# Performance work log

Measured on AMD Instinct MI355X. Metric: run time of the kernel, lower is better.

The kernel has to match this reference:

```python
import jax, jax.numpy as jnp
import numpy as np

TAU = 2.0
EPS = 1e-5
NUM_HEADS = 8


def _atan_surrogate(alpha):
    @jax.custom_vjp
    def f(x):
        return (x >= 0).astype(x.dtype)
    def fwd(x):
        return f(x), x
    def bwd(x, g):
        d = (alpha / 2.0) / (1.0 + (jnp.pi / 2.0 * alpha * x) ** 2)
        return (g * d,)
    f.defvjp(fwd, bwd)
    return f


def _sigmoid_surrogate(alpha):
    @jax.custom_vjp
    def f(x):
        return (x >= 0).astype(x.dtype)
    def fwd(x):
        return f(x), x
    def bwd(x, g):
        s = jax.nn.sigmoid(alpha * x)
        return (g * alpha * s * (1.0 - s),)
    f.defvjp(fwd, bwd)
    return f


spike_atan5 = _atan_surrogate(5.0)   # surrogate.ATan(alpha=5.0)
spike_sig4 = _sigmoid_surrogate(4.0)  # spikingjelly default surrogate.Sigmoid(alpha=4.0)


def lif(x, spike_fn, v_th=1.0):
    """LIF over leading time dim. decay_input=True, v_reset=0 (hard reset), detach_reset=True.
    x: [T, ...] membrane input. Returns spikes [T, ...]."""
    def step(v, xt):
        v = v + (xt - v) / TAU
        s = spike_fn(v - v_th)
        v = v * (1.0 - jax.lax.stop_gradient(s))  # hard reset to 0, detached
        return v, s
    _, spikes = jax.lax.scan(step, jnp.zeros_like(x[0]), x)
    return spikes


def conv1x1(x, w, b=None):
    # x: [T,B,Cin,H,W], w: [Cout,Cin]
    y = jnp.einsum('tbihw,oi->tbohw', x, w)
    if b is not None:
        y = y + b[None, None, :, None, None]
    return y


def bn(x, p):
    # eval-mode BatchNorm2d; p: [4,C] = (gamma, beta, running_mean, running_var)
    g, be, m, v = p[0], p[1], p[2], p[3]
    sc = g / jnp.sqrt(v + EPS)
    return (x - m[None, None, :, None, None]) * sc[None, None, :, None, None] + be[None, None, :, None, None]


def setup_inputs() -> dict:
    key = jax.random.key(0)
    T, B, C, H, W = 4, 16, 512, 16, 16
    hid = 4 * C
    ks = jax.random.split(key, 16)

    def w(k, o, i):
        return (jax.random.normal(k, (o, i), dtype=jnp.float32) / np.sqrt(i)).astype(jnp.float32)

    def make_bn(k, c):
        k1, k2, k3, k4 = jax.random.split(k, 4)
        g = 1.0 + 0.1 * jax.random.normal(k1, (c,), dtype=jnp.float32)
        be = 0.1 * jax.random.normal(k2, (c,), dtype=jnp.float32)
        m = 0.1 * jax.random.normal(k3, (c,), dtype=jnp.float32)
        v = 1.0 + 0.1 * jax.random.uniform(k4, (c,), dtype=jnp.float32)
        return jnp.stack([g, be, m, v])

    return {
        'x': jax.random.normal(ks[0], (T, B, C, H, W), dtype=jnp.float32),
        'q_w': w(ks[1], C, C), 'k_w': w(ks[2], C, C), 'v_w': w(ks[3], C, C),
        'proj_w': w(ks[4], C, C),
        'proj_b': 0.01 * jax.random.normal(ks[5], (C,), dtype=jnp.float32),
        'fc1_w': w(ks[6], hid, C),
        'fc1_b': 0.01 * jax.random.normal(ks[7], (hid,), dtype=jnp.float32),
        'fc2_w': w(ks[8], C, hid),
        'fc2_b': 0.01 * jax.random.normal(ks[9], (C,), dtype=jnp.float32),
        'q_bn': make_bn(ks[10], C), 'k_bn': make_bn(ks[11], C), 'v_bn': make_bn(ks[12], C),
        'proj_bn': make_bn(ks[13], C), 'fc1_bn': make_bn(ks[14], hid), 'fc2_bn': make_bn(ks[15], C),
    }


def reference(x, q_w, k_w, v_w, proj_w, proj_b, fc1_w, fc1_b, fc2_w, fc2_b,
              q_bn, k_bn, v_bn, proj_bn, fc1_bn, fc2_bn):
    T, B, C, H, W = x.shape
    N = H * W
    Ch = C // NUM_HEADS

    # ---- MS_SSA_Conv ----
    identity = x
    xs = lif(x, spike_sig4)                               # shortcut_lif (default surrogate)
    q = lif(bn(conv1x1(xs, q_w), q_bn), spike_atan5)      # [T,B,C,H,W] spikes
    k = lif(bn(conv1x1(xs, k_w), k_bn), spike_atan5)
    v = lif(bn(conv1x1(xs, v_w), v_bn), spike_atan5)

    def to_heads(t):  # [T,B,C,H,W] -> [T,B,h,N,Ch]
        return t.reshape(T, B, NUM_HEADS, Ch, N).transpose(0, 1, 2, 4, 3)

    qh, kh, vh = to_heads(q), to_heads(k), to_heads(v)
    kv = (kh * vh).sum(axis=3, keepdims=True)             # [T,B,h,1,Ch] linear attention reduce
    kv = lif(kv, spike_sig4, v_th=0.5)                    # talking_heads_lif
    att = qh * kv                                         # [T,B,h,N,Ch]
    att = att.transpose(0, 1, 2, 4, 3).reshape(T, B, C, H, W)
    x_attn = bn(conv1x1(att, proj_w, proj_b), proj_bn) + identity

    # ---- MS_MLP_Conv (hidden = 4*C != C, so no mid residual) ----
    idm = x_attn
    h = lif(x_attn, spike_atan5)
    h = bn(conv1x1(h, fc1_w, fc1_b), fc1_bn)              # [T,B,4C,H,W]
    h = lif(h, spike_atan5)
    h = bn(conv1x1(h, fc2_w, fc2_b), fc2_bn)
    out = h + idm
    return out, vh
```

## Files before the change

### kernel.cpp

```cpp
#include <hip/hip_runtime.h>
#include <stdint.h>

#pragma clang fp contract(off)

typedef int i32x4 __attribute__((ext_vector_type(4)));
typedef float f32x4 __attribute__((ext_vector_type(4)));
typedef unsigned char u8;

#define T_   4
#define B_   16
#define C_   512
#define HID_ 2048
#define NPIX 256
#define Z_   64

constexpr size_t OFF_AB      = 0;
constexpr size_t OFF_PRESUM  = 65536;
constexpr size_t OFF_MASK    = OFF_PRESUM + 524288;
constexpr size_t OFF_WD      = OFF_MASK + 65536;
constexpr size_t SZ_QKVD = 1536*512;
constexpr size_t SZ_PD   = 512*512;
constexpr size_t SZ_F1D  = 2048*512;
constexpr size_t SZ_F2D  = 512*2048;
constexpr size_t OFF_QKV1 = OFF_WD;
constexpr size_t OFF_QKV0 = OFF_QKV1 + SZ_QKVD;
constexpr size_t OFF_P1   = OFF_QKV0 + SZ_QKVD;
constexpr size_t OFF_P0   = OFF_P1 + SZ_PD;
constexpr size_t OFF_F11  = OFF_P0 + SZ_PD;
constexpr size_t OFF_F10  = OFF_F11 + SZ_F1D;
constexpr size_t OFF_F21  = OFF_F10 + SZ_F1D;
constexpr size_t OFF_F20  = OFF_F21 + SZ_F2D;
constexpr size_t SPKB8    = (size_t)64*256*512;
constexpr size_t OFF_SPK_A   = (OFF_F20 + SZ_F2D + 255) & ~(size_t)255;
constexpr size_t OFF_SPK_QKV = OFF_SPK_A + SPKB8;
constexpr size_t OFF_SPK_E   = OFF_SPK_QKV + 3*SPKB8;
constexpr size_t OFF_H2      = OFF_SPK_E + SPKB8;

__global__ __launch_bounds__(256) void prep_quant_kernel(
        const float* __restrict__ q_w, const float* __restrict__ k_w,
        const float* __restrict__ v_w, const float* __restrict__ p_w,
        const float* __restrict__ f1_w, const float* __restrict__ f2_w,
        const float* __restrict__ q_bn, const float* __restrict__ k_bn,
        const float* __restrict__ v_bn, const float* __restrict__ p_bn,
        const float* __restrict__ f1_bn, const float* __restrict__ f2_bn,
        const float* __restrict__ p_b, const float* __restrict__ f1_b,
        const float* __restrict__ f2_b, char* ws) {
    int wv = threadIdx.x >> 6, lane = threadIdx.x & 63;
    int r = blockIdx.x * 4 + wv;
    const float* wsrc; const float* bn; const float* bias;
    char *d1, *d0; int Cin, Cn, o;
    if (r < 512)        { o=r;       wsrc=q_w  + (size_t)o*512;  bn=q_bn;  bias=nullptr; Cin=512;  Cn=512;
                          d1=ws+OFF_QKV1+(size_t)r*512;      d0=ws+OFF_QKV0+(size_t)r*512; }
    else if (r < 1024)  { o=r-512;   wsrc=k_w  + (size_t)o*512;  bn=k_bn;  bias=nullptr; Cin=512;  Cn=512;
                          d1=ws+OFF_QKV1+(size_t)r*512;      d0=ws+OFF_QKV0+(size_t)r*512; }
    else if (r < 1536)  { o=r-1024;  wsrc=v_w  + (size_t)o*512;  bn=v_bn;  bias=nullptr; Cin=512;  Cn=512;
                          d1=ws+OFF_QKV1+(size_t)r*512;      d0=ws+OFF_QKV0+(size_t)r*512; }
    else if (r < 2048)  { o=r-1536;  wsrc=p_w  + (size_t)o*512;  bn=p_bn;  bias=p_b;     Cin=512;  Cn=512;
                          d1=ws+OFF_P1+(size_t)o*512;        d0=ws+OFF_P0+(size_t)o*512; }
    else if (r < 4096)  { o=r-2048;  wsrc=f1_w + (size_t)o*512;  bn=f1_bn; bias=f1_b;    Cin=512;  Cn=2048;
                          d1=ws+OFF_F11+(size_t)o*512;       d0=ws+OFF_F10+(size_t)o*512; }
    else if (r < 4608)  { o=r-4096;  wsrc=f2_w + (size_t)o*2048; bn=f2_bn; bias=f2_b;    Cin=2048; Cn=512;
                          d1=ws+OFF_F21+(size_t)o*2048;      d0=ws+OFF_F20+(size_t)o*2048; }
    else return;

    float mx = 0.0f;
    for (int c = lane; c < Cin; c += 64) mx = fmaxf(mx, fabsf(wsrc[c]));
    #pragma unroll
    for (int off = 32; off; off >>= 1) mx = fmaxf(mx, __shfl_xor(mx, off));

    int E; float mant = frexpf(mx, &E);
    int sh = (ldexpf(mant, 15) > 32639.0f) ? (14 - E) : (15 - E);
    if (mx == 0.0f) sh = 0;
    float S = ldexpf(1.0f, sh);

    for (int c = lane; c < Cin; c += 64) {
        int q = __float2int_rn(wsrc[c] * S);
        int t0 = ((q + 128) & 255) - 128;
        int t1 = (q - t0) >> 8;
        d0[c] = (char)t0;
        d1[c] = (char)t1;
    }
    if (lane == 0) {
        float g  = bn[o];
        float be = bn[Cn + o];
        float m  = bn[2 * Cn + o];
        float vv = bn[3 * Cn + o];
        float sc = g / sqrtf(vv + 1e-5f);
        float bv = bias ? bias[o] : 0.0f;
        float2* ab = (float2*)(ws + OFF_AB) + r;
        *ab = make_float2(sc * ldexpf(1.0f, -sh), (bv - m) * sc + be);
    }
}

__global__ __launch_bounds__(256) void lif_transpose_kernel(
        const float* __restrict__ y, u8* __restrict__ spk, int Cf) {
    __shared__ __align__(16) u8 tile[256 * 80];
    int b  = blockIdx.z;
    int c0 = blockIdx.y * 64;
    int n0 = blockIdx.x * 64;
    int tid = threadIdx.x;
    int nn = tid & 63;
    int cg = tid >> 6;
    size_t tstride = (size_t)B_ * Cf * NPIX;
    for (int e = 0; e < 16; ++e) {
        int ci = cg * 16 + e;
        size_t base = ((size_t)b * Cf + c0 + ci) * NPIX + n0 + nn;
        float v = 0.0f;
        #pragma unroll
        for (int t = 0; t < T_; ++t) {
            float x = y[base + (size_t)t * tstride];
            v = v + (x - v) * 0.5f;
            u8 s = 0;
            if (v >= 1.0f) { s = 1; v = 0.0f; }
            tile[(t * 64 + nn) * 80 + ci] = s;
        }
    }
    __syncthreads();
    int t = tid >> 6, n2 = tid & 63;
    const u8* srow = &tile[(t * 64 + n2) * 80];
    u8* drow = spk + ((size_t)((t * B_ + b) * NPIX) + n0 + n2) * Cf + c0;
    #pragma unroll
    for (int kk = 0; kk < 4; ++kk)
        *(uint4*)(drow + kk * 16) = *(const uint4*)(srow + kk * 16);
}

__global__ void kv_presum_kernel(const u8* __restrict__ qkv, int* __restrict__ presum4) {
    int z  = blockIdx.x >> 2;
    int nq = blockIdx.x & 3;
    int tid = threadIdx.x;
    if (tid >= 128) return;
    const uint* base = (const uint*)(qkv + (size_t)z * NPIX * 1536 + (size_t)nq * 64 * 1536);
    int s0 = 0, s1 = 0, s2 = 0, s3 = 0;
    for (int n = 0; n < 64; ++n) {
        uint a = base[n * 384 + 128 + tid];
        uint b = base[n * 384 + 256 + tid];
        uint c = a & b;
        s0 += c & 1; s1 += (c >> 8) & 1; s2 += (c >> 16) & 1; s3 += (c >> 24) & 1;
    }
    int o = ((nq * Z_ + z) << 9) + 4 * tid;
    presum4[o] = s0; presum4[o + 1] = s1; presum4[o + 2] = s2; presum4[o + 3] = s3;
}

__global__ void kv_lif_mask_kernel(const int* __restrict__ presum4, u8* __restrict__ mask) {
    int i = blockIdx.x * 256 + threadIdx.x;
    int b = i >> 9, c = i & (C_ - 1);
    float v = 0.0f;
    #pragma unroll
    for (int t = 0; t < T_; ++t) {
        int z = t * B_ + b;
        int s = presum4[(z << 9) + c] + presum4[((Z_ + z) << 9) + c]
              + presum4[((2 * Z_ + z) << 9) + c] + presum4[((3 * Z_ + z) << 9) + c];
        float x = (float)s;
        v = v + (x - v) * 0.5f;
        u8 m = 0;
        if (v >= 0.5f) { m = 0xFF; v = 0.0f; }
        mask[(z << 9) + c] = m;
    }
}

__global__ void att_apply_kernel(const u8* __restrict__ qkv, const u8* __restrict__ mask,
                                 u8* __restrict__ att) {
    size_t i = (size_t)blockIdx.x * 256 + threadIdx.x;
    int z   = (int)(i >> 14);
    int rem = (int)(i & 16383);
    int n   = rem >> 6;
    int c8  = rem & 63;
    uint2 qv = *(const uint2*)(qkv + ((size_t)z * NPIX + n) * 1536 + c8 * 8);
    uint2 mv = *(const uint2*)(mask + (size_t)z * C_ + c8 * 8);
    uint2 r;
    r.x = qv.x & mv.x;
    r.y = qv.y & mv.y;
    *(uint2*)(att + ((size_t)z * NPIX + n) * 512 + c8 * 8) = r;
}

__global__ __launch_bounds__(512, 4) void gemm_fused_kernel(
        const u8* __restrict__ S,
        const char* __restrict__ Wd1,
        const char* __restrict__ Wd0,
        const float2* __restrict__ AB,
        const float* res,
        float* yout,
        u8* spkout,
        float* vhout,
        int Cin, int Cout, int mode) {
    __shared__ __align__(16) char lds[49152];
    float* ldsf = (float*)lds;
    const int tid  = threadIdx.x;
    const int lane = tid & 63;
    const int w    = tid >> 6;
    const int oh   = w >> 2;
    const int zz   = w & 3;
    const int r15 = lane & 15, quad = lane >> 4;
    const int id = blockIdx.x;
    const int b  = (id >> 2) & 15;
    const int o0 = (id >> 6) * 64;
    const int p0 = (id & 3) * 64;
    const int zt = zz * B_ + b;

    i32x4 acc1[2][4], acc2[2][4];
    #pragma unroll
    for (int a = 0; a < 2; ++a)
        #pragma unroll
        for (int c = 0; c < 4; ++c) {
            acc1[a][c] = (i32x4){0, 0, 0, 0};
            acc2[a][c] = (i32x4){0, 0, 0, 0};
        }

    const int srow = lane >> 2;
    const int sj   = lane & 3;

    const char* ssrc[3];
    int sdst[3];
    #pragma unroll
    for (int e = 0; e < 3; ++e) {
        int g = w * 3 + e;
        if (g < 4) {
            int m = g * 16 + srow;
            ssrc[e] = Wd1 + (size_t)(o0 + m) * Cin + ((sj ^ ((m >> 1) & 3)) << 4);
            sdst[e] = g * 1024;
        } else if (g < 8) {
            int m = (g - 4) * 16 + srow;
            ssrc[e] = Wd0 + (size_t)(o0 + m) * Cin + ((sj ^ ((m >> 1) & 3)) << 4);
            sdst[e] = 4096 + (g - 4) * 1024;
        } else {
            int r = (g - 8) * 16 + srow;
            int t = r >> 6, p = r & 63;
            ssrc[e] = (const char*)S + ((size_t)((t * B_ + b) * NPIX + p0 + p)) * Cin
                      + ((sj ^ ((r >> 1) & 3)) << 4);
            sdst[e] = 8192 + (g - 8) * 1024;
        }
    }

    auto stage = [&](int k0, int st) {
        #pragma unroll
        for (int e = 0; e < 3; ++e) {
            __builtin_amdgcn_global_load_lds(
                (const __attribute__((address_space(1))) void*)(uintptr_t)(const void*)(ssrc[e] + k0),
                (__attribute__((address_space(3))) void*)(uintptr_t)(void*)(lds + st * 24576 + sdst[e]),
                16, 0, 0);
        }
    };

    int offA[2], offL[2], offB[4];
    #pragma unroll
    for (int mt = 0; mt < 2; ++mt) {
        int m = oh * 32 + mt * 16 + r15;
        offA[mt] = m * 64 + ((quad ^ ((m >> 1) & 3)) << 4);
        offL[mt] = 4096 + offA[mt];
    }
    #pragma unroll
    for (int nt = 0; nt < 4; ++nt) {
        int r = zz * 64 + nt * 16 + r15;
        offB[nt] = 8192 + r * 64 + ((quad ^ ((r >> 1) & 3)) << 4);
    }

    auto compute = [&](int bufbase) {
        i32x4 af[2], al[2], bf[4];
        #pragma unroll
        for (int mt = 0; mt < 2; ++mt) {
            af[mt] = *(const i32x4*)(lds + bufbase + offA[mt]);
            al[mt] = *(const i32x4*)(lds + bufbase + offL[mt]);
        }
        #pragma unroll
        for (int nt = 0; nt < 4; ++nt)
            bf[nt] = *(const i32x4*)(lds + bufbase + offB[nt]);
        #pragma unroll
        for (int mt = 0; mt < 2; ++mt)
            #pragma unroll
            for (int nt = 0; nt < 4; ++nt) {
                acc1[mt][nt] = __builtin_amdgcn_mfma_i32_16x16x64_i8(af[mt], bf[nt], acc1[mt][nt], 0, 0, 0);
                acc2[mt][nt] = __builtin_amdgcn_mfma_i32_16x16x64_i8(al[mt], bf[nt], acc2[mt][nt], 0, 0, 0);
            }
    };

    const int nIter = Cin >> 6;
    stage(0, 0);
    int k = 64;
    for (int i = 0; i < nIter; i += 2) {
        __syncthreads();
        if (i + 1 < nIter) stage(k, 1);
        k += 64;
        compute(0);
        __syncthreads();
        if (i + 2 < nIter) stage(k, 0);
        k += 64;
        compute(24576);
    }

    f32x4 yv[2][4];
    #pragma unroll
    for (int mt = 0; mt < 2; ++mt) {
        int obl = o0 + oh * 32 + mt * 16 + quad * 4;
        float av[4], bv[4];
        #pragma unroll
        for (int r = 0; r < 4; ++r) {
            float2 abv = AB[obl + r];
            av[r] = abv.x; bv[r] = abv.y;
        }
        #pragma unroll
        for (int nt = 0; nt < 4; ++nt) {
            int p = p0 + nt * 16 + r15;
            #pragma unroll
            for (int r = 0; r < 4; ++r) {
                int qi = (acc1[mt][nt][r] << 8) + acc2[mt][nt][r];
                float val = fmaf((float)qi, av[r], bv[r]);
                if (mode != 0) {
                    size_t idx = ((size_t)zt * Cout + obl + r) * NPIX + p;
                    val += res[idx];
                }
                yv[mt][nt][r] = val;
            }
        }
    }
    if (mode != 0) {
        #pragma unroll
        for (int mt = 0; mt < 2; ++mt) {
            int ob = o0 + oh * 32 + mt * 16 + quad * 4;
            #pragma unroll
            for (int nt = 0; nt < 4; ++nt) {
                int p = p0 + nt * 16 + r15;
                #pragma unroll
                for (int r = 0; r < 4; ++r)
                    yout[((size_t)zt * Cout + ob + r) * NPIX + p] = yv[mt][nt][r];
            }
        }
    }
    if (mode != 2) {
        __syncthreads();
        const int o2 = tid & 63;
        const int pj = tid >> 6;
        const bool dovh = (vhout != nullptr) && (o0 >= 1024);
        const int hsec = (o0 - 1024) >> 6;
        #pragma unroll
        for (int ph = 0; ph < 4; ++ph) {
            #pragma unroll
            for (int mt = 0; mt < 2; ++mt) {
                int ol = oh * 32 + mt * 16 + quad * 4;
                #pragma unroll
                for (int r = 0; r < 4; ++r)
                    ldsf[zz * 1088 + (ol + r) * 17 + r15] = yv[mt][ph][r];
            }
            __syncthreads();
            u8 sp[4][2];
            #pragma unroll
            for (int jj = 0; jj < 2; ++jj) {
                int p = pj * 2 + jj;
                float v = 0.0f;
                #pragma unroll
                for (int t = 0; t < T_; ++t) {
                    float x = ldsf[t * 1088 + o2 * 17 + p];
                    v = v + (x - v) * 0.5f;
                    u8 s = 0;
                    if (v >= 1.0f) { s = 1; v = 0.0f; }
                    sp[t][jj] = s;
                }
            }
            #pragma unroll
            for (int t = 0; t < T_; ++t)
                #pragma unroll
                for (int jj = 0; jj < 2; ++jj) {
                    int p = p0 + ph * 16 + pj * 2 + jj;
                    spkout[((size_t)((t * B_ + b) * NPIX + p)) * Cout + o0 + o2] = sp[t][jj];
                    if (dovh)
                        vhout[((((size_t)(t * B_ + b)) * 8 + hsec) * NPIX + p) * 64 + o2] =
                            sp[t][jj] ? 1.0f : 0.0f;
                }
            __syncthreads();
        }
    }
}

extern "C" void kernel_launch(void* const* d_in, const int* in_sizes, int n_in,
                              void* d_out, int out_size, void* d_ws, size_t ws_size,
                              hipStream_t stream) {
    (void)in_sizes; (void)n_in; (void)out_size; (void)ws_size;
    const float* x       = (const float*)d_in[0];
    const float* q_w     = (const float*)d_in[1];
    const float* k_w     = (const float*)d_in[2];
    const float* v_w     = (const float*)d_in[3];
    const float* proj_w  = (const float*)d_in[4];
    const float* proj_b  = (const float*)d_in[5];
    const float* fc1_w   = (const float*)d_in[6];
    const float* fc1_b   = (const float*)d_in[7];
    const float* fc2_w   = (const float*)d_in[8];
    const float* fc2_b   = (const float*)d_in[9];
    const float* q_bn    = (const float*)d_in[10];
    const float* k_bn    = (const float*)d_in[11];
    const float* v_bn    = (const float*)d_in[12];
    const float* proj_bn = (const float*)d_in[13];
    const float* fc1_bn  = (const float*)d_in[14];
    const float* fc2_bn  = (const float*)d_in[15];

    char* ws = (char*)d_ws;
    float2* abb   = (float2*)(ws + OFF_AB);
    int*   presum4 = (int*)(ws + OFF_PRESUM);
    u8*    maskp   = (u8*)(ws + OFF_MASK);
    const char *qkv1 = ws + OFF_QKV1, *qkv0 = ws + OFF_QKV0;
    const char *p1 = ws + OFF_P1,   *p0d = ws + OFF_P0;
    const char *f11 = ws + OFF_F11, *f10 = ws + OFF_F10;
    const char *f21 = ws + OFF_F21, *f20 = ws + OFF_F20;
    u8* spkA   = (u8*)(ws + OFF_SPK_A);
    u8* spkQKV = (u8*)(ws + OFF_SPK_QKV);
    u8* spkE   = (u8*)(ws + OFF_SPK_E);
    u8* h2     = (u8*)(ws + OFF_H2);

    float* out1 = (float*)d_out;
    float* out2 = out1 + 8388608;
    float* x_attn = out1;

    prep_quant_kernel<<<1152, 256, 0, stream>>>(q_w, k_w, v_w, proj_w, fc1_w, fc2_w,
                                                q_bn, k_bn, v_bn, proj_bn, fc1_bn, fc2_bn,
                                                proj_b, fc1_b, fc2_b, ws);

    dim3 gLT(4, 8, 16);

    lif_transpose_kernel<<<gLT, 256, 0, stream>>>(x, spkA, C_);

    gemm_fused_kernel<<<24 * 64, 512, 0, stream>>>(spkA, qkv1, qkv0, abb,
                                                   nullptr, nullptr, spkQKV, out2, C_, 1536, 0);

    kv_presum_kernel<<<256, 256, 0, stream>>>(spkQKV, presum4);
    kv_lif_mask_kernel<<<32, 256, 0, stream>>>(presum4, maskp);
    att_apply_kernel<<<4096, 256, 0, stream>>>(spkQKV, maskp, spkA);

    gemm_fused_kernel<<<8 * 64, 512, 0, stream>>>(spkA, p1, p0d, abb + 1536,
                                                  x, x_attn, spkE, nullptr, C_, C_, 1);

    gemm_fused_kernel<<<32 * 64, 512, 0, stream>>>(spkE, f11, f10, abb + 2048,
                                                   nullptr, nullptr, h2, nullptr, C_, HID_, 0);

    gemm_fused_kernel<<<8 * 64, 512, 0, stream>>>(h2, f21, f20, abb + 4096,
                                                  x_attn, out1, nullptr, nullptr, HID_, C_, 2);
}
```

Measured before the change: 295.2 us.

## Load spike B-operand directly into registers and shrink LDS staging

The int8 spike activation tile (B operand) is now read straight from global memory into registers with a register double buffer. LDS holds only the two weight planes, so shared memory drops from 48KB to 16KB per block, which may allow more resident blocks. Block index decomposition is reordered so consecutive blocks share the same batch and differ in output-channel tile, aiming for better L2 reuse of activations. The cost is that the two waves sharing a pixel tile each fetch the same B data, and global-load latency is now exposed directly to the MFMA loop.

```diff
diff --git a/kernel.cpp b/kernel.cpp
--- a/kernel.cpp
+++ b/kernel.cpp
@@ -183,7 +183,7 @@
         u8* spkout,
         float* vhout,
         int Cin, int Cout, int mode) {
-    __shared__ __align__(16) char lds[49152];
+    __shared__ __align__(16) char lds[16384];
     float* ldsf = (float*)lds;
     const int tid  = threadIdx.x;
     const int lane = tid & 63;
@@ -192,9 +192,13 @@
     const int zz   = w & 3;
     const int r15 = lane & 15, quad = lane >> 4;
     const int id = blockIdx.x;
-    const int b  = (id >> 2) & 15;
-    const int o0 = (id >> 6) * 64;
-    const int p0 = (id & 3) * 64;
+    const int nOy = Cout >> 6;
+    const int px  = id & 3;
+    const int rest = id >> 2;
+    const int oy  = rest % nOy;
+    const int b   = rest / nOy;
+    const int o0 = oy * 64;
+    const int p0 = px * 64;
     const int zt = zz * B_ + b;
 
     i32x4 acc1[2][4], acc2[2][4];
@@ -209,61 +213,53 @@
     const int srow = lane >> 2;
     const int sj   = lane & 3;
 
-    const char* ssrc[3];
-    int sdst[3];
-    #pragma unroll
-    for (int e = 0; e < 3; ++e) {
-        int g = w * 3 + e;
+    const char* ssrc;
+    int sdst;
+    {
+        int g = w;
         if (g < 4) {
             int m = g * 16 + srow;
-            ssrc[e] = Wd1 + (size_t)(o0 + m) * Cin + ((sj ^ ((m >> 1) & 3)) << 4);
-            sdst[e] = g * 1024;
-        } else if (g < 8) {
+            ssrc = Wd1 + (size_t)(o0 + m) * Cin + ((sj ^ ((m >> 1) & 3)) << 4);
+        } else {
             int m = (g - 4) * 16 + srow;
-            ssrc[e] = Wd0 + (size_t)(o0 + m) * Cin + ((sj ^ ((m >> 1) & 3)) << 4);
-            sdst[e] = 4096 + (g - 4) * 1024;
-        } else {
-            int r = (g - 8) * 16 + srow;
-            int t = r >> 6, p = r & 63;
-            ssrc[e] = (const char*)S + ((size_t)((t * B_ + b) * NPIX + p0 + p)) * Cin
-                      + ((sj ^ ((r >> 1) & 3)) << 4);
-            sdst[e] = 8192 + (g - 8) * 1024;
-        }
+            ssrc = Wd0 + (size_t)(o0 + m) * Cin + ((sj ^ ((m >> 1) & 3)) << 4);
+        }
+        sdst = g * 1024;
     }
 
     auto stage = [&](int k0, int st) {
-        #pragma unroll
-        for (int e = 0; e < 3; ++e) {
-            __builtin_amdgcn_global_load_lds(
-                (const __attribute__((address_space(1))) void*)(uintptr_t)(const void*)(ssrc[e] + k0),
-                (__attribute__((address_space(3))) void*)(uintptr_t)(void*)(lds + st * 24576 + sdst[e]),
-                16, 0, 0);
-        }
+        __builtin_amdgcn_global_load_lds(
+            (const __attribute__((address_space(1))) void*)(uintptr_t)(const void*)(ssrc + k0),
+            (__attribute__((address_space(3))) void*)(uintptr_t)(void*)(lds + st * 8192 + sdst),
+            16, 0, 0);
     };
 
-    int offA[2], offL[2], offB[4];
+    int offA[2], offL[2];
     #pragma unroll
     for (int mt = 0; mt < 2; ++mt) {
         int m = oh * 32 + mt * 16 + r15;
         offA[mt] = m * 64 + ((quad ^ ((m >> 1) & 3)) << 4);
         offL[mt] = 4096 + offA[mt];
     }
-    #pragma unroll
-    for (int nt = 0; nt < 4; ++nt) {
-        int r = zz * 64 + nt * 16 + r15;
-        offB[nt] = 8192 + r * 64 + ((quad ^ ((r >> 1) & 3)) << 4);
-    }
-
-    auto compute = [&](int bufbase) {
-        i32x4 af[2], al[2], bf[4];
+
+    const char* bsrc[4];
+    #pragma unroll
+    for (int nt = 0; nt < 4; ++nt)
+        bsrc[nt] = (const char*)S + ((size_t)(zt * NPIX + p0 + nt * 16 + r15)) * Cin + quad * 16;
+
+    auto loadB = [&](int k0, i32x4* bf) {
+        #pragma unroll
+        for (int nt = 0; nt < 4; ++nt)
+            bf[nt] = *(const i32x4*)(bsrc[nt] + k0);
+    };
+
+    auto compute = [&](int bufbase, const i32x4* bf) {
+        i32x4 af[2], al[2];
         #pragma unroll
         for (int mt = 0; mt < 2; ++mt) {
             af[mt] = *(const i32x4*)(lds + bufbase + offA[mt]);
             al[mt] = *(const i32x4*)(lds + bufbase + offL[mt]);
         }
-        #pragma unroll
-        for (int nt = 0; nt < 4; ++nt)
-            bf[nt] = *(const i32x4*)(lds + bufbase + offB[nt]);
         #pragma unroll
         for (int mt = 0; mt < 2; ++mt)
             #pragma unroll
@@ -274,17 +270,19 @@
     };
 
     const int nIter = Cin >> 6;
+    i32x4 bcur[4], bnxt[4];
     stage(0, 0);
+    loadB(0, bcur);
     int k = 64;
     for (int i = 0; i < nIter; i += 2) {
         __syncthreads();
-        if (i + 1 < nIter) stage(k, 1);
+        if (i + 1 < nIter) { stage(k, 1); loadB(k, bnxt); }
         k += 64;
-        compute(0);
+        compute(0, bcur);
         __syncthreads();
-        if (i + 2 < nIter) stage(k, 0);
+        if (i + 2 < nIter) { stage(k, 0); loadB(k, bcur); }
         k += 64;
-        compute(24576);
+        compute(8192, bnxt);
     }
 
     f32x4 yv[2][4];
```

New measurement: 401.5 us. 36.0% more time.

## Remap GEMM waves so each thread holds all timesteps, LIF in registers

Applied to the files above, without the earlier changes.

Reassigns the four waves per output-half from timestep slices to pixel slices, so every thread accumulates all four timesteps for its outputs. The LIF recurrence over time then runs entirely in registers instead of going through an LDS transpose with several block barriers. Spikes are packed four channels per 32-bit store and the vh output is written as float4. The price is less coalesced output writes, since the packed stores stride across pixels, and different register pressure.

```diff
diff --git a/kernel.cpp b/kernel.cpp
--- a/kernel.cpp
+++ b/kernel.cpp
@@ -184,24 +184,22 @@
         float* vhout,
         int Cin, int Cout, int mode) {
     __shared__ __align__(16) char lds[49152];
-    float* ldsf = (float*)lds;
     const int tid  = threadIdx.x;
     const int lane = tid & 63;
     const int w    = tid >> 6;
     const int oh   = w >> 2;
-    const int zz   = w & 3;
+    const int pq   = w & 3;
     const int r15 = lane & 15, quad = lane >> 4;
     const int id = blockIdx.x;
     const int b  = (id >> 2) & 15;
     const int o0 = (id >> 6) * 64;
     const int p0 = (id & 3) * 64;
-    const int zt = zz * B_ + b;
-
-    i32x4 acc1[2][4], acc2[2][4];
-    #pragma unroll
-    for (int a = 0; a < 2; ++a)
-        #pragma unroll
-        for (int c = 0; c < 4; ++c) {
+
+    i32x4 acc1[4][2], acc2[4][2];
+    #pragma unroll
+    for (int a = 0; a < 4; ++a)
+        #pragma unroll
+        for (int c = 0; c < 2; ++c) {
             acc1[a][c] = (i32x4){0, 0, 0, 0};
             acc2[a][c] = (i32x4){0, 0, 0, 0};
         }
@@ -249,9 +247,9 @@
         offL[mt] = 4096 + offA[mt];
     }
     #pragma unroll
-    for (int nt = 0; nt < 4; ++nt) {
-        int r = zz * 64 + nt * 16 + r15;
-        offB[nt] = 8192 + r * 64 + ((quad ^ ((r >> 1) & 3)) << 4);
+    for (int z = 0; z < 4; ++z) {
+        int r = z * 64 + pq * 16 + r15;
+        offB[z] = 8192 + r * 64 + ((quad ^ ((r >> 1) & 3)) << 4);
     }
 
     auto compute = [&](int bufbase) {
@@ -262,14 +260,14 @@
             al[mt] = *(const i32x4*)(lds + bufbase + offL[mt]);
         }
         #pragma unroll
-        for (int nt = 0; nt < 4; ++nt)
-            bf[nt] = *(const i32x4*)(lds + bufbase + offB[nt]);
-        #pragma unroll
-        for (int mt = 0; mt < 2; ++mt)
+        for (int z = 0; z < 4; ++z)
+            bf[z] = *(const i32x4*)(lds + bufbase + offB[z]);
+        #pragma unroll
+        for (int z = 0; z < 4; ++z)
             #pragma unroll
-            for (int nt = 0; nt < 4; ++nt) {
-                acc1[mt][nt] = __builtin_amdgcn_mfma_i32_16x16x64_i8(af[mt], bf[nt], acc1[mt][nt], 0, 0, 0);
-                acc2[mt][nt] = __builtin_amdgcn_mfma_i32_16x16x64_i8(al[mt], bf[nt], acc2[mt][nt], 0, 0, 0);
+            for (int mt = 0; mt < 2; ++mt) {
+                acc1[z][mt] = __builtin_amdgcn_mfma_i32_16x16x64_i8(af[mt], bf[z], acc1[z][mt], 0, 0, 0);
+                acc2[z][mt] = __builtin_amdgcn_mfma_i32_16x16x64_i8(al[mt], bf[z], acc2[z][mt], 0, 0, 0);
             }
     };
 
@@ -287,85 +285,79 @@
         compute(24576);
     }
 
-    f32x4 yv[2][4];
-    #pragma unroll
-    for (int mt = 0; mt < 2; ++mt) {
-        int obl = o0 + oh * 32 + mt * 16 + quad * 4;
-        float av[4], bv[4];
+    const int p = p0 + pq * 16 + r15;
+    float av[2][4], bc[2][4];
+    #pragma unroll
+    for (int mt = 0; mt < 2; ++mt)
         #pragma unroll
         for (int r = 0; r < 4; ++r) {
-            float2 abv = AB[obl + r];
-            av[r] = abv.x; bv[r] = abv.y;
-        }
-        #pragma unroll
-        for (int nt = 0; nt < 4; ++nt) {
-            int p = p0 + nt * 16 + r15;
+            float2 abv = AB[o0 + oh * 32 + mt * 16 + quad * 4 + r];
+            av[mt][r] = abv.x; bc[mt][r] = abv.y;
+        }
+    f32x4 yv[4][2];
+    #pragma unroll
+    for (int z = 0; z < 4; ++z) {
+        int zt = z * B_ + b;
+        #pragma unroll
+        for (int mt = 0; mt < 2; ++mt) {
+            int obl = o0 + oh * 32 + mt * 16 + quad * 4;
             #pragma unroll
             for (int r = 0; r < 4; ++r) {
-                int qi = (acc1[mt][nt][r] << 8) + acc2[mt][nt][r];
-                float val = fmaf((float)qi, av[r], bv[r]);
-                if (mode != 0) {
-                    size_t idx = ((size_t)zt * Cout + obl + r) * NPIX + p;
-                    val += res[idx];
-                }
-                yv[mt][nt][r] = val;
+                int qi = (acc1[z][mt][r] << 8) + acc2[z][mt][r];
+                float val = fmaf((float)qi, av[mt][r], bc[mt][r]);
+                if (mode != 0)
+                    val += res[((size_t)zt * Cout + obl + r) * NPIX + p];
+                yv[z][mt][r] = val;
             }
         }
     }
     if (mode != 0) {
         #pragma unroll
-        for (int mt = 0; mt < 2; ++mt) {
-            int ob = o0 + oh * 32 + mt * 16 + quad * 4;
+        for (int z = 0; z < 4; ++z) {
+            int zt = z * B_ + b;
             #pragma unroll
-            for (int nt = 0; nt < 4; ++nt) {
-                int p = p0 + nt * 16 + r15;
+            for (int mt = 0; mt < 2; ++mt) {
+                int obl = o0 + oh * 32 + mt * 16 + quad * 4;
                 #pragma unroll
                 for (int r = 0; r < 4; ++r)
-                    yout[((size_t)zt * Cout + ob + r) * NPIX + p] = yv[mt][nt][r];
+                    yout[((size_t)zt * Cout + obl + r) * NPIX + p] = yv[z][mt][r];
             }
         }
     }
     if (mode != 2) {
-        __syncthreads();
-        const int o2 = tid & 63;
-        const int pj = tid >> 6;
         const bool dovh = (vhout != nullptr) && (o0 >= 1024);
         const int hsec = (o0 - 1024) >> 6;
         #pragma unroll
-        for (int ph = 0; ph < 4; ++ph) {
+        for (int mt = 0; mt < 2; ++mt) {
+            int obl = o0 + oh * 32 + mt * 16 + quad * 4;
+            uint pk0 = 0, pk1 = 0, pk2 = 0, pk3 = 0;
+            f32x4 vh0, vh1, vh2, vh3;
             #pragma unroll
-            for (int mt = 0; mt < 2; ++mt) {
-                int ol = oh * 32 + mt * 16 + quad * 4;
-                #pragma unroll
-                for (int r = 0; r < 4; ++r)
-                    ldsf[zz * 1088 + (ol + r) * 17 + r15] = yv[mt][ph][r];
+            for (int r = 0; r < 4; ++r) {
+                float v = 0.0f;
+                uint s0, s1, s2, s3;
+                float x0 = yv[0][mt][r];
+                v = v + (x0 - v) * 0.5f; s0 = 0; if (v >= 1.0f) { s0 = 1; v = 0.0f; }
+                float x1 = yv[1][mt][r];
+                v = v + (x1 - v) * 0.5f; s1 = 0; if (v >= 1.0f) { s1 = 1; v = 0.0f; }
+                float x2 = yv[2][mt][r];
+                v = v + (x2 - v) * 0.5f; s2 = 0; if (v >= 1.0f) { s2 = 1; v = 0.0f; }
+                float x3 = yv[3][mt][r];
+                v = v + (x3 - v) * 0.5f; s3 = 0; if (v >= 1.0f) { s3 = 1; v = 0.0f; }
+                pk0 |= s0 << (8 * r); pk1 |= s1 << (8 * r);
+                pk2 |= s2 << (8 * r); pk3 |= s3 << (8 * r);
+                vh0[r] = (float)s0; vh1[r] = (float)s1;
+                vh2[r] = (float)s2; vh3[r] = (float)s3;
             }
-            __syncthreads();
-            u8 sp[4][2];
+            uint pks[4] = {pk0, pk1, pk2, pk3};
+            f32x4 vhs[4] = {vh0, vh1, vh2, vh3};
             #pragma unroll
-            for (int jj = 0; jj < 2; ++jj) {
-                int p = pj * 2 + jj;
-                float v = 0.0f;
-                #pragma unroll
-                for (int t = 0; t < T_; ++t) {
-                    float x = ldsf[t * 1088 + o2 * 17 + p];
-                    v = v + (x - v) * 0.5f;
-                    u8 s = 0;
-                    if (v >= 1.0f) { s = 1; v = 0.0f; }
-                    sp[t][jj] = s;
-                }
+            for (int t = 0; t < 4; ++t) {
+                *(uint*)(spkout + ((size_t)((t * B_ + b) * NPIX + p)) * Cout + obl) = pks[t];
+                if (dovh)
+                    *(f32x4*)(vhout + ((((size_t)(t * B_ + b)) * 8 + hsec) * NPIX + p) * 64
+                              + (obl - o0)) = vhs[t];
             }
-            #pragma unroll
-            for (int t = 0; t < T_; ++t)
-                #pragma unroll
-                for (int jj = 0; jj < 2; ++jj) {
-                    int p = p0 + ph * 16 + pj * 2 + jj;
-                    spkout[((size_t)((t * B_ + b) * NPIX + p)) * Cout + o0 + o2] = sp[t][jj];
-                    if (dovh)
-                        vhout[((((size_t)(t * B_ + b)) * 8 + hsec) * NPIX + p) * 64 + o2] =
-                            sp[t][jj] ? 1.0f : 0.0f;
-                }
-            __syncthreads();
         }
     }
 }
```

After: 301.7 us. +2.2%, slower.
